# Optimization experiments

Hardware: AMD Instinct MI355X
Metric: run time of the kernel (lower is better)

The kernel has to match this reference:

```python
import jax, jax.numpy as jnp
import numpy as np

K = 16        # top-K nodes per sample (from self.K)
C_IN = 2048   # conv1 in_channels
C_OUT = 256   # conv1 out_channels
D_OUT = 512   # fc1 out_features (in_features = K*C_OUT = 4096)


def setup_inputs() -> dict:
    key = jax.random.key(0)
    k0, k1, k2 = jax.random.split(key, 3)
    N, W, H = 128, 16, 16
    sounds = jax.random.normal(k0, (N, C_IN, W, H), dtype=jnp.float32)
    conv_w = jax.random.normal(k1, (C_OUT, C_IN), dtype=jnp.float32) * 0.02
    conv_b = jnp.zeros((C_OUT,), jnp.float32)
    fc_w = jax.random.normal(k2, (D_OUT, K * C_OUT), dtype=jnp.float32) * 0.02
    fc_b = jnp.zeros((D_OUT,), jnp.float32)
    return {"sounds": sounds, "conv_w": conv_w, "conv_b": conv_b,
            "fc_w": fc_w, "fc_b": fc_b}


def _dynamic_lnorm(rows, cols):
    """Symmetric-normalized spatial-affinity graph over the K nodes.

    Reconstructs the (undefined) Graph_Init.Dynamic_Lnorm: adjacency from
    spatial proximity of node coordinates, D^{-1/2} A D^{-1/2}.
    rows, cols: [N, K] int -> Lnorm [N, K, K] float.
    """
    coords = jnp.stack([rows, cols], axis=-1).astype(jnp.float32)  # [N,K,2]
    d2 = jnp.sum((coords[:, :, None, :] - coords[:, None, :, :]) ** 2, axis=-1)
    A = jnp.exp(-d2 / (2.0 * K))          # soft adjacency, self-loop weight 1
    dinv = jax.lax.rsqrt(jnp.sum(A, axis=-1))
    return A * dinv[:, :, None] * dinv[:, None, :]


def reference(sounds, conv_w, conv_b, fc_w, fc_b):
    N, C, W, H = sounds.shape
    # channel-sum saliency map (the original adds all channels into Fre)
    fre = jnp.sum(sounds, axis=1)                       # [N, W, H]
    feat = fre.reshape(N, W * H)
    _, idx = jax.lax.top_k(feat, K)                     # [N, K] descending (== sort[:, :K])
    # faithful replication of the original (off-by-one) coordinate math
    rows = jnp.where(idx < H, idx // H, idx // H - 1)   # [N, K]
    cols = jnp.where(idx % H == 0, H - 1, idx % H - 1)  # [N, K]
    # gather node features: [N, K, C]
    nodes = sounds[jnp.arange(N)[:, None], :, rows, cols]
    lnorm = _dynamic_lnorm(rows, cols)                  # [N, K, K]
    # conv1x1 on [K, C, 1, 1] == per-node linear 2048 -> 256, then ReLU
    x = jax.nn.relu(jnp.einsum('nkc,oc->nko', nodes, conv_w) + conv_b)  # [N,K,256]
    # graph aggregation: Lnorm @ x per sample
    y = jnp.einsum('nij,njo->nio', lnorm, x)            # [N, K, 256]
    # flatten nodes and apply fc1 (4096 -> 512)
    return y.reshape(N, K * C_OUT) @ fc_w.T + fc_b      # [N, 512]
```

## Files before the change

### kernel.cpp

```cpp
#include <hip/hip_runtime.h>
#include <math.h>

typedef __attribute__((ext_vector_type(8))) short short8;
typedef __attribute__((ext_vector_type(4))) float f32x4;
typedef unsigned short ushort;
typedef unsigned int uint;

#define NB   128
#define CIN  2048
#define PP   256
#define KK   16
#define CO   256
#define DO   512

#define WS_PARTIAL 0
#define WS_POS     1048576
#define WS_LNORM   1050624
#define WS_NODES   1083392
#define WS_WB      3180544
#define WS_XPART   3442688
#define WS_Y       7636992

__device__ __forceinline__ ushort f2bf(float f) {
    uint u = __builtin_bit_cast(uint, f);
    u += 0x7fffu + ((u >> 16) & 1u);
    return (ushort)(u >> 16);
}

__global__ __launch_bounds__(256) void k_prep(const float* __restrict__ conv_w,
                                              ushort* __restrict__ Wb,
                                              const float* __restrict__ fcb,
                                              float* __restrict__ out) {
    int b = blockIdx.x, t = threadIdx.x;
    if (b < 512) {
        int idx = (b * 256 + t) * 4;
        float4 v = *(const float4*)(conv_w + idx);
        uint2 u;
        u.x = (uint)f2bf(v.x) | ((uint)f2bf(v.y) << 16);
        u.y = (uint)f2bf(v.z) | ((uint)f2bf(v.w) << 16);
        *(uint2*)(Wb + idx) = u;
    } else {
        int i = (b - 512) * 256 + t;
        out[i] = fcb[i & 511];
    }
}

__global__ __launch_bounds__(256) void k_reduce(const float* __restrict__ snd,
                                                float* __restrict__ partial) {
    int n = blockIdx.x, chunk = blockIdx.y, t = threadIdx.x;
    int sub = t >> 6, p4 = t & 63;
    const float4* base = (const float4*)(snd + (size_t)n * CIN * PP
                                         + (size_t)(chunk * 256 + sub * 64) * PP) + p4;
    float4 acc = make_float4(0.f, 0.f, 0.f, 0.f);
#pragma unroll 4
    for (int c = 0; c < 64; ++c) {
        float4 v = base[c * 64];
        acc.x += v.x; acc.y += v.y; acc.z += v.z; acc.w += v.w;
    }
    ((float4*)(partial + (size_t)(n * 32 + chunk * 4 + sub) * 256))[p4] = acc;
}

__global__ __launch_bounds__(256) void k_topk_lnorm(const float* __restrict__ partial,
                                                    int* __restrict__ pos,
                                                    float* __restrict__ lnorm) {
    int n = blockIdx.x, t = threadIdx.x;
    int lane = t & 63, wv = t >> 6;
    __shared__ float wval[4];
    __shared__ int   widx[4];
    __shared__ int   sel[16];
    __shared__ float rr[16], cc[16], dinv[16];
    __shared__ float Ash[256];

    float v = 0.f;
#pragma unroll 8
    for (int j = 0; j < 32; ++j) v += partial[(size_t)(n * 32 + j) * 256 + t];

    for (int k = 0; k < 16; ++k) {
        float bv = v; int bi = t;
#pragma unroll
        for (int off = 32; off > 0; off >>= 1) {
            float ov = __shfl_xor(bv, off, 64);
            int   oi = __shfl_xor(bi, off, 64);
            if (ov > bv || (ov == bv && oi < bi)) { bv = ov; bi = oi; }
        }
        if (lane == 0) { wval[wv] = bv; widx[wv] = bi; }
        __syncthreads();
        float best = wval[0]; int besti = widx[0];
#pragma unroll
        for (int w = 1; w < 4; ++w) {
            float ww = wval[w]; int wi = widx[w];
            if (ww > best || (ww == best && wi < besti)) { best = ww; besti = wi; }
        }
        if (t == besti) v = -INFINITY;
        if (t == 0) sel[k] = besti;
        __syncthreads();
    }

    if (t < 16) {
        int idx = sel[t];
        int r = (idx < 16) ? (idx >> 4) : ((idx >> 4) - 1);
        int c = ((idx & 15) == 0) ? 15 : ((idx & 15) - 1);
        pos[n * 16 + t] = r * 16 + c;
        rr[t] = (float)r; cc[t] = (float)c;
    }
    __syncthreads();
    {
        int i = t >> 4, j = t & 15;
        float dr = rr[i] - rr[j], dc = cc[i] - cc[j];
        Ash[t] = expf(-(dr * dr + dc * dc) * (1.0f / 32.0f));
    }
    __syncthreads();
    if (t < 16) {
        float srow = 0.f;
#pragma unroll
        for (int j = 0; j < 16; ++j) srow += Ash[t * 16 + j];
        dinv[t] = rsqrtf(srow);
    }
    __syncthreads();
    {
        int i = t >> 4, j = t & 15;
        lnorm[(size_t)n * 256 + t] = Ash[t] * dinv[i] * dinv[j];
    }
}

__global__ __launch_bounds__(256) void k_gather(const float* __restrict__ snd,
                                                const int* __restrict__ pos,
                                                ushort* __restrict__ nodes) {
    int n = blockIdx.x, cg = blockIdx.y, t = threadIdx.x;
    int w = t >> 6, l = t & 63;
    __shared__ int lpos[16];
    __shared__ ushort Nsh[16][34];
    if (t < 16) lpos[t] = pos[n * 16 + t];
    __syncthreads();

    int p = lpos[l & 15];
    int srclane = p >> 2;
    int comp = p & 3;

    const float4* rowbase = (const float4*)(snd + (size_t)n * CIN * PP
                                            + (size_t)(cg * 32 + w * 8) * PP);
    float4 vv[8];
#pragma unroll
    for (int cc = 0; cc < 8; ++cc) vv[cc] = rowbase[(size_t)cc * 64 + l];

#pragma unroll
    for (int cc = 0; cc < 8; ++cc) {
        float s0 = __shfl(vv[cc].x, srclane, 64);
        float s1 = __shfl(vv[cc].y, srclane, 64);
        float s2 = __shfl(vv[cc].z, srclane, 64);
        float s3 = __shfl(vv[cc].w, srclane, 64);
        float val = (comp & 2) ? ((comp & 1) ? s3 : s2)
                               : ((comp & 1) ? s1 : s0);
        if (l < 16) Nsh[l][w * 8 + cc] = f2bf(val);
    }
    __syncthreads();

    int kk = t >> 4, u = t & 15;
    uint pv = (uint)Nsh[kk][u * 2] | ((uint)Nsh[kk][u * 2 + 1] << 16);
    ((uint*)(nodes + (size_t)(n * 16 + kk) * 2048 + cg * 32))[u] = pv;
}

__global__ __launch_bounds__(256) void k_conv(const ushort* __restrict__ nodes,
                                              const ushort* __restrict__ Wb,
                                              float* __restrict__ Xpart) {
    int bm = blockIdx.x, bo = blockIdx.y, kc = blockIdx.z, t = threadIdx.x;
    int w = t >> 6, l = t & 63;
    int lm = l & 15, quad = l >> 4;
    __shared__ ushort As[64 * 72];
    __shared__ ushort Bs[64 * 72];
    f32x4 acc[4] = {{0.f,0.f,0.f,0.f},{0.f,0.f,0.f,0.f},{0.f,0.f,0.f,0.f},{0.f,0.f,0.f,0.f}};
    int m0 = bm * 64, o0 = bo * 64;
    int srow = t >> 3, seg = t & 7;
    const ushort* ard = As + (w * 16 + lm) * 72 + quad * 8;
    const ushort* brd = Bs + lm * 72 + quad * 8;

    for (int c0 = kc * 256; c0 < kc * 256 + 256; c0 += 64) {
#pragma unroll
        for (int i = 0; i < 2; ++i) {
            int r = i * 32 + srow;
            *(uint4*)(As + r * 72 + seg * 8) =
                *(const uint4*)(nodes + (size_t)(m0 + r) * 2048 + c0 + seg * 8);
            *(uint4*)(Bs + r * 72 + seg * 8) =
                *(const uint4*)(Wb + (size_t)(o0 + r) * 2048 + c0 + seg * 8);
        }
        __syncthreads();
#pragma unroll
        for (int ks = 0; ks < 2; ++ks) {
            short8 af = *(const short8*)(ard + ks * 32);
#pragma unroll
            for (int ot = 0; ot < 4; ++ot) {
                short8 bf = *(const short8*)(brd + ot * 16 * 72 + ks * 32);
                acc[ot] = __builtin_amdgcn_mfma_f32_16x16x32_bf16(af, bf, acc[ot], 0, 0, 0);
            }
        }
        __syncthreads();
    }

    float* Xp = Xpart + (size_t)kc * 524288;
#pragma unroll
    for (int ot = 0; ot < 4; ++ot) {
        int o = o0 + ot * 16 + lm;
#pragma unroll
        for (int r = 0; r < 4; ++r) {
            int m = m0 + w * 16 + quad * 4 + r;
            Xp[(size_t)m * 256 + o] = acc[ot][r];
        }
    }
}

__global__ __launch_bounds__(256) void k_xmix(const float* __restrict__ Xpart,
                                              const float* __restrict__ bias,
                                              const float* __restrict__ lnorm,
                                              float* __restrict__ Y) {
    int n = blockIdx.x, o = threadIdx.x;
    __shared__ float ln[256];
    ln[o] = lnorm[(size_t)n * 256 + o];
    float b = bias[o];
    __syncthreads();
    float xv[16];
#pragma unroll
    for (int j = 0; j < 16; ++j) {
        size_t off = (size_t)(n * 16 + j) * 256 + o;
        float s = b;
#pragma unroll
        for (int kc = 0; kc < 8; ++kc) s += Xpart[(size_t)kc * 524288 + off];
        xv[j] = fmaxf(s, 0.0f);
    }
#pragma unroll
    for (int i = 0; i < 16; ++i) {
        float a = 0.f;
#pragma unroll
        for (int j = 0; j < 16; ++j) a += ln[i * 16 + j] * xv[j];
        Y[(size_t)n * 4096 + i * 256 + o] = a;
    }
}

__global__ __launch_bounds__(256) void k_fc(const float* __restrict__ Y,
                                            const float* __restrict__ Fw,
                                            float* __restrict__ out) {
    int bn = blockIdx.x, bd = blockIdx.y, bk = blockIdx.z, t = threadIdx.x;
    int to = t & 15, tm = t >> 4;
    __shared__ float Ys[16 * 34];
    __shared__ float Fs[16 * 68];
    float acc[2][4] = {};
    int n0 = bn * 32, d0 = bd * 64, kbase = bk * 256;
    for (int c0 = kbase; c0 < kbase + 256; c0 += 16) {
#pragma unroll
        for (int i = 0; i < 2; ++i) {
            int e = i * 256 + t;
            int m = e >> 4, k = e & 15;
            Ys[k * 34 + m] = Y[(size_t)(n0 + m) * 4096 + c0 + k];
        }
#pragma unroll
        for (int i = 0; i < 4; ++i) {
            int e = i * 256 + t;
            int d = e >> 4, k = e & 15;
            Fs[k * 68 + d] = Fw[(size_t)(d0 + d) * 4096 + c0 + k];
        }
        __syncthreads();
#pragma unroll
        for (int k = 0; k < 16; ++k) {
            float2 a = *(const float2*)&Ys[k * 34 + tm * 2];
            float4 b = *(const float4*)&Fs[k * 68 + to * 4];
            acc[0][0] += a.x * b.x; acc[0][1] += a.x * b.y;
            acc[0][2] += a.x * b.z; acc[0][3] += a.x * b.w;
            acc[1][0] += a.y * b.x; acc[1][1] += a.y * b.y;
            acc[1][2] += a.y * b.z; acc[1][3] += a.y * b.w;
        }
        __syncthreads();
    }
#pragma unroll
    for (int i = 0; i < 2; ++i) {
        int nn = n0 + tm * 2 + i;
#pragma unroll
        for (int j = 0; j < 4; ++j) {
            int d = d0 + to * 4 + j;
            atomicAdd(&out[(size_t)nn * 512 + d], acc[i][j]);
        }
    }
}

extern "C" void kernel_launch(void* const* d_in, const int* in_sizes, int n_in,
                              void* d_out, int out_size, void* d_ws, size_t ws_size,
                              hipStream_t stream) {
    const float* snd    = (const float*)d_in[0];
    const float* conv_w = (const float*)d_in[1];
    const float* conv_b = (const float*)d_in[2];
    const float* fc_w   = (const float*)d_in[3];
    const float* fc_b   = (const float*)d_in[4];
    float* out = (float*)d_out;
    float* ws  = (float*)d_ws;

    float*  partial = ws + WS_PARTIAL;
    int*    pos     = (int*)(ws + WS_POS);
    float*  lnorm   = ws + WS_LNORM;
    ushort* nodes   = (ushort*)(ws + WS_NODES);
    ushort* Wb      = (ushort*)(ws + WS_WB);
    float*  Xpart   = ws + WS_XPART;
    float*  Y       = ws + WS_Y;

    k_prep<<<768, 256, 0, stream>>>(conv_w, Wb, fc_b, out);
    k_reduce<<<dim3(128, 8), 256, 0, stream>>>(snd, partial);
    k_topk_lnorm<<<128, 256, 0, stream>>>(partial, pos, lnorm);
    k_gather<<<dim3(128, 64), 256, 0, stream>>>(snd, pos, nodes);
    k_conv<<<dim3(32, 4, 8), 256, 0, stream>>>(nodes, Wb, Xpart);
    k_xmix<<<128, 256, 0, stream>>>(Xpart, conv_b, lnorm, Y);
    k_fc<<<dim3(4, 8, 16), 256, 0, stream>>>(Y, fc_w, out);
}
```

Before: 474.4 us.

## Compute 1x1 conv for all positions fused with channel-sum pass, then select top-K

Replaces the separate reduce, gather and split-K conv kernels with one kernel that streams the input once, accumulating the channel-sum saliency while running a bf16 MFMA GEMM of the conv weights against every spatial position. After top-K, a selection kernel picks the 16 chosen positions' conv outputs, then applies bias, ReLU and the graph mix. This removes the second read of the large input tensor that the gather needed. In exchange it does 16x more conv FLOPs and writes a 32 MB full conv-output buffer. The weights are stored XOR-swizzled to avoid LDS bank conflicts.

After: 432.8 us. -8.8%, faster.

```diff
diff --git a/kernel.cpp b/kernel.cpp
--- a/kernel.cpp
+++ b/kernel.cpp
@@ -13,13 +13,12 @@
 #define CO   256
 #define DO   512
 
-#define WS_PARTIAL 0
-#define WS_POS     1048576
-#define WS_LNORM   1050624
-#define WS_NODES   1083392
-#define WS_WB      3180544
-#define WS_XPART   3442688
-#define WS_Y       7636992
+#define WS_FRE   0
+#define WS_POS   32768
+#define WS_LNORM 34816
+#define WS_WG    67584
+#define WS_XALL  329728
+#define WS_Y     8718336
 
 __device__ __forceinline__ ushort f2bf(float f) {
     uint u = __builtin_bit_cast(uint, f);
@@ -28,39 +27,127 @@
 }
 
 __global__ __launch_bounds__(256) void k_prep(const float* __restrict__ conv_w,
-                                              ushort* __restrict__ Wb,
+                                              ushort* __restrict__ Wg,
                                               const float* __restrict__ fcb,
                                               float* __restrict__ out) {
     int b = blockIdx.x, t = threadIdx.x;
     if (b < 512) {
-        int idx = (b * 256 + t) * 4;
-        float4 v = *(const float4*)(conv_w + idx);
+        int e0 = (b * 256 + t) * 4;
+        int o  = e0 >> 11;
+        int c  = e0 & 2047;
+        int x  = ((o ^ (o >> 3)) & 7) << 3;
+        int cs = c ^ x;
+        float4 v = *(const float4*)(conv_w + e0);
         uint2 u;
         u.x = (uint)f2bf(v.x) | ((uint)f2bf(v.y) << 16);
         u.y = (uint)f2bf(v.z) | ((uint)f2bf(v.w) << 16);
-        *(uint2*)(Wb + idx) = u;
+        *(uint2*)(Wg + (size_t)o * 2048 + cs) = u;
     } else {
         int i = (b - 512) * 256 + t;
         out[i] = fcb[i & 511];
     }
 }
 
-__global__ __launch_bounds__(256) void k_reduce(const float* __restrict__ snd,
-                                                float* __restrict__ partial) {
-    int n = blockIdx.x, chunk = blockIdx.y, t = threadIdx.x;
-    int sub = t >> 6, p4 = t & 63;
-    const float4* base = (const float4*)(snd + (size_t)n * CIN * PP
-                                         + (size_t)(chunk * 256 + sub * 64) * PP) + p4;
-    float4 acc = make_float4(0.f, 0.f, 0.f, 0.f);
-#pragma unroll 4
-    for (int c = 0; c < 64; ++c) {
-        float4 v = base[c * 64];
-        acc.x += v.x; acc.y += v.y; acc.z += v.z; acc.w += v.w;
-    }
-    ((float4*)(partial + (size_t)(n * 32 + chunk * 4 + sub) * 256))[p4] = acc;
-}
-
-__global__ __launch_bounds__(256) void k_topk_lnorm(const float* __restrict__ partial,
+__global__ __launch_bounds__(256) void k_convall(const float* __restrict__ snd,
+                                                 const ushort* __restrict__ Wg,
+                                                 float* __restrict__ Xall,
+                                                 float* __restrict__ fre) {
+    int n = blockIdx.x, pb = blockIdx.y, t = threadIdx.x;
+    int w = t >> 6, l = t & 63, lm = l & 15, quad = l >> 4;
+    __shared__ ushort As[256 * 64];
+    __shared__ float  Bs[64 * 66];
+
+    f32x4 acc[4][4] = {};
+    float4 facc = make_float4(0.f, 0.f, 0.f, 0.f);
+
+    int sg = t >> 4, pos4 = t & 15;
+    const float* sbase = snd + (size_t)n * (CIN * PP) + pb * 64;
+
+    int xsw[4], abase[4];
+#pragma unroll
+    for (int ot = 0; ot < 4; ++ot) {
+        int o = w * 64 + ot * 16 + lm;
+        xsw[ot] = (o ^ (o >> 3)) & 7;
+        abase[ot] = o * 64;
+    }
+
+    for (int it = 0; it < 32; ++it) {
+        int c0 = it * 64;
+#pragma unroll
+        for (int i = 0; i < 8; ++i) {
+            int oo = i * 32 + (t >> 3);
+            int seg = t & 7;
+            const ushort* src = Wg + (size_t)oo * 2048 + c0 + seg * 8;
+            ushort* dst = As + oo * 64 + seg * 8;
+            __builtin_amdgcn_global_load_lds(
+                (const __attribute__((address_space(1))) uint*)src,
+                (__attribute__((address_space(3))) uint*)dst, 16, 0, 0);
+        }
+        float4 sv[4];
+#pragma unroll
+        for (int rc = 0; rc < 4; ++rc) {
+            int cl = rc * 16 + sg;
+            sv[rc] = *(const float4*)(sbase + (size_t)(c0 + cl) * PP + pos4 * 4);
+        }
+#pragma unroll
+        for (int rc = 0; rc < 4; ++rc) {
+            facc.x += sv[rc].x; facc.y += sv[rc].y;
+            facc.z += sv[rc].z; facc.w += sv[rc].w;
+            int cl = rc * 16 + sg;
+            float* wp = Bs + cl * 66 + pos4 * 4;
+            *(float2*)wp       = make_float2(sv[rc].x, sv[rc].y);
+            *(float2*)(wp + 2) = make_float2(sv[rc].z, sv[rc].w);
+        }
+        __syncthreads();
+#pragma unroll
+        for (int ks = 0; ks < 2; ++ks) {
+            short8 af[4];
+#pragma unroll
+            for (int ot = 0; ot < 4; ++ot) {
+                int seg = (ks * 4 + quad) ^ xsw[ot];
+                af[ot] = *(const short8*)(As + abase[ot] + seg * 8);
+            }
+#pragma unroll
+            for (int pt = 0; pt < 4; ++pt) {
+                const float* bp = Bs + (ks * 32 + quad * 8) * 66 + pt * 16 + lm;
+                uint u0 = (uint)f2bf(bp[0])   | ((uint)f2bf(bp[66])  << 16);
+                uint u1 = (uint)f2bf(bp[132]) | ((uint)f2bf(bp[198]) << 16);
+                uint u2 = (uint)f2bf(bp[264]) | ((uint)f2bf(bp[330]) << 16);
+                uint u3 = (uint)f2bf(bp[396]) | ((uint)f2bf(bp[462]) << 16);
+                short8 bf = __builtin_bit_cast(short8, make_uint4(u0, u1, u2, u3));
+#pragma unroll
+                for (int ot = 0; ot < 4; ++ot)
+                    acc[ot][pt] = __builtin_amdgcn_mfma_f32_16x16x32_bf16(
+                        af[ot], bf, acc[ot][pt], 0, 0, 0);
+            }
+        }
+        __syncthreads();
+    }
+
+    float* xo = Xall + (size_t)n * 256 * 256;
+#pragma unroll
+    for (int ot = 0; ot < 4; ++ot) {
+#pragma unroll
+        for (int pt = 0; pt < 4; ++pt) {
+            int pos = pb * 64 + pt * 16 + lm;
+            int o   = w * 64 + ot * 16 + quad * 4;
+            *(float4*)(xo + (size_t)pos * 256 + o) =
+                make_float4(acc[ot][pt][0], acc[ot][pt][1], acc[ot][pt][2], acc[ot][pt][3]);
+        }
+    }
+
+    float* scr = (float*)As;
+    *(float4*)(scr + sg * 64 + pos4 * 4) = facc;
+    __syncthreads();
+    if (t < 64) {
+        float s = 0.f;
+#pragma unroll
+        for (int g = 0; g < 16; ++g) s += scr[g * 64 + t];
+        fre[n * 256 + pb * 64 + t] = s;
+    }
+}
+
+__global__ __launch_bounds__(256) void k_topk_lnorm(const float* __restrict__ fre,
                                                     int* __restrict__ pos,
                                                     float* __restrict__ lnorm) {
     int n = blockIdx.x, t = threadIdx.x;
@@ -71,9 +158,7 @@
     __shared__ float rr[16], cc[16], dinv[16];
     __shared__ float Ash[256];
 
-    float v = 0.f;
-#pragma unroll 8
-    for (int j = 0; j < 32; ++j) v += partial[(size_t)(n * 32 + j) * 256 + t];
+    float v = fre[n * 256 + t];
 
     for (int k = 0; k < 16; ++k) {
         float bv = v; int bi = t;
@@ -123,108 +208,22 @@
     }
 }
 
-__global__ __launch_bounds__(256) void k_gather(const float* __restrict__ snd,
-                                                const int* __restrict__ pos,
-                                                ushort* __restrict__ nodes) {
-    int n = blockIdx.x, cg = blockIdx.y, t = threadIdx.x;
-    int w = t >> 6, l = t & 63;
-    __shared__ int lpos[16];
-    __shared__ ushort Nsh[16][34];
-    if (t < 16) lpos[t] = pos[n * 16 + t];
-    __syncthreads();
-
-    int p = lpos[l & 15];
-    int srclane = p >> 2;
-    int comp = p & 3;
-
-    const float4* rowbase = (const float4*)(snd + (size_t)n * CIN * PP
-                                            + (size_t)(cg * 32 + w * 8) * PP);
-    float4 vv[8];
-#pragma unroll
-    for (int cc = 0; cc < 8; ++cc) vv[cc] = rowbase[(size_t)cc * 64 + l];
-
-#pragma unroll
-    for (int cc = 0; cc < 8; ++cc) {
-        float s0 = __shfl(vv[cc].x, srclane, 64);
-        float s1 = __shfl(vv[cc].y, srclane, 64);
-        float s2 = __shfl(vv[cc].z, srclane, 64);
-        float s3 = __shfl(vv[cc].w, srclane, 64);
-        float val = (comp & 2) ? ((comp & 1) ? s3 : s2)
-                               : ((comp & 1) ? s1 : s0);
-        if (l < 16) Nsh[l][w * 8 + cc] = f2bf(val);
-    }
-    __syncthreads();
-
-    int kk = t >> 4, u = t & 15;
-    uint pv = (uint)Nsh[kk][u * 2] | ((uint)Nsh[kk][u * 2 + 1] << 16);
-    ((uint*)(nodes + (size_t)(n * 16 + kk) * 2048 + cg * 32))[u] = pv;
-}
-
-__global__ __launch_bounds__(256) void k_conv(const ushort* __restrict__ nodes,
-                                              const ushort* __restrict__ Wb,
-                                              float* __restrict__ Xpart) {
-    int bm = blockIdx.x, bo = blockIdx.y, kc = blockIdx.z, t = threadIdx.x;
-    int w = t >> 6, l = t & 63;
-    int lm = l & 15, quad = l >> 4;
-    __shared__ ushort As[64 * 72];
-    __shared__ ushort Bs[64 * 72];
-    f32x4 acc[4] = {{0.f,0.f,0.f,0.f},{0.f,0.f,0.f,0.f},{0.f,0.f,0.f,0.f},{0.f,0.f,0.f,0.f}};
-    int m0 = bm * 64, o0 = bo * 64;
-    int srow = t >> 3, seg = t & 7;
-    const ushort* ard = As + (w * 16 + lm) * 72 + quad * 8;
-    const ushort* brd = Bs + lm * 72 + quad * 8;
-
-    for (int c0 = kc * 256; c0 < kc * 256 + 256; c0 += 64) {
-#pragma unroll
-        for (int i = 0; i < 2; ++i) {
-            int r = i * 32 + srow;
-            *(uint4*)(As + r * 72 + seg * 8) =
-                *(const uint4*)(nodes + (size_t)(m0 + r) * 2048 + c0 + seg * 8);
-            *(uint4*)(Bs + r * 72 + seg * 8) =
-                *(const uint4*)(Wb + (size_t)(o0 + r) * 2048 + c0 + seg * 8);
-        }
-        __syncthreads();
-#pragma unroll
-        for (int ks = 0; ks < 2; ++ks) {
-            short8 af = *(const short8*)(ard + ks * 32);
-#pragma unroll
-            for (int ot = 0; ot < 4; ++ot) {
-                short8 bf = *(const short8*)(brd + ot * 16 * 72 + ks * 32);
-                acc[ot] = __builtin_amdgcn_mfma_f32_16x16x32_bf16(af, bf, acc[ot], 0, 0, 0);
-            }
-        }
-        __syncthreads();
-    }
-
-    float* Xp = Xpart + (size_t)kc * 524288;
-#pragma unroll
-    for (int ot = 0; ot < 4; ++ot) {
-        int o = o0 + ot * 16 + lm;
-#pragma unroll
-        for (int r = 0; r < 4; ++r) {
-            int m = m0 + w * 16 + quad * 4 + r;
-            Xp[(size_t)m * 256 + o] = acc[ot][r];
-        }
-    }
-}
-
-__global__ __launch_bounds__(256) void k_xmix(const float* __restrict__ Xpart,
+__global__ __launch_bounds__(256) void k_xsel(const float* __restrict__ Xall,
+                                              const int* __restrict__ pos,
                                               const float* __restrict__ bias,
                                               const float* __restrict__ lnorm,
                                               float* __restrict__ Y) {
     int n = blockIdx.x, o = threadIdx.x;
     __shared__ float ln[256];
+    __shared__ int lp[16];
     ln[o] = lnorm[(size_t)n * 256 + o];
+    if (o < 16) lp[o] = pos[n * 16 + o];
     float b = bias[o];
     __syncthreads();
     float xv[16];
 #pragma unroll
     for (int j = 0; j < 16; ++j) {
-        size_t off = (size_t)(n * 16 + j) * 256 + o;
-        float s = b;
-#pragma unroll
-        for (int kc = 0; kc < 8; ++kc) s += Xpart[(size_t)kc * 524288 + off];
-        xv[j] = fmaxf(s, 0.0f);
+        xv[j] = fmaxf(Xall[((size_t)n * 256 + lp[j]) * 256 + o] + b, 0.0f);
     }
 #pragma unroll
     for (int i = 0; i < 16; ++i) {
@@ -291,19 +290,16 @@
     float* out = (float*)d_out;
     float* ws  = (float*)d_ws;
 
-    float*  partial = ws + WS_PARTIAL;
-    int*    pos     = (int*)(ws + WS_POS);
-    float*  lnorm   = ws + WS_LNORM;
-    ushort* nodes   = (ushort*)(ws + WS_NODES);
-    ushort* Wb      = (ushort*)(ws + WS_WB);
-    float*  Xpart   = ws + WS_XPART;
-    float*  Y       = ws + WS_Y;
-
-    k_prep<<<768, 256, 0, stream>>>(conv_w, Wb, fc_b, out);
-    k_reduce<<<dim3(128, 8), 256, 0, stream>>>(snd, partial);
-    k_topk_lnorm<<<128, 256, 0, stream>>>(partial, pos, lnorm);
-    k_gather<<<dim3(128, 64), 256, 0, stream>>>(snd, pos, nodes);
-    k_conv<<<dim3(32, 4, 8), 256, 0, stream>>>(nodes, Wb, Xpart);
-    k_xmix<<<128, 256, 0, stream>>>(Xpart, conv_b, lnorm, Y);
+    float*  fre   = ws + WS_FRE;
+    int*    pos   = (int*)(ws + WS_POS);
+    float*  lnorm = ws + WS_LNORM;
+    ushort* Wg    = (ushort*)(ws + WS_WG);
+    float*  Xall  = ws + WS_XALL;
+    float*  Y     = ws + WS_Y;
+
+    k_prep<<<768, 256, 0, stream>>>(conv_w, Wg, fc_b, out);
+    k_convall<<<dim3(128, 4), 256, 0, stream>>>(snd, Wg, Xall, fre);
+    k_topk_lnorm<<<128, 256, 0, stream>>>(fre, pos, lnorm);
+    k_xsel<<<128, 256, 0, stream>>>(Xall, pos, conv_b, lnorm, Y);
     k_fc<<<dim3(4, 8, 16), 256, 0, stream>>>(Y, fc_w, out);
 }
```
